# Kernel tuning notes

Measured on AMD Instinct MI355X. Metric: run time of the kernel, lower is better.

The kernel has to match this reference:

```python
import jax, jax.numpy as jnp
import numpy as np

B, C, H, W = 4, 512, 64, 64
CI = C // 8  # q/k channels in spatial attention
EPS = 1e-5


def _conv3(x, w):
    # 3x3 same-padding conv, NCHW / OIHW, no bias (BN follows)
    return jax.lax.conv_general_dilated(x, w, (1, 1), 'SAME',
                                        dimension_numbers=('NCHW', 'OIHW', 'NCHW'))


def _bn_relu(y, g, b, m, v):
    scale = (g / jnp.sqrt(v + EPS))[None, :, None, None]
    return jax.nn.relu((y - m[None, :, None, None]) * scale + b[None, :, None, None])


def setup_inputs() -> dict:
    ks = jax.random.split(jax.random.key(0), 16)
    f = lambda i, sh, s=0.05: jax.random.normal(ks[i], sh, dtype=jnp.float32) * s
    u = lambda i, sh: jax.random.uniform(ks[i], sh, dtype=jnp.float32) + 0.5
    d = {'x': f(0, (B, C, H, W), 1.0)}
    # spatial branch: conv-bn-relu, attention (q/k/v 1x1 convs + alpha), conv-bn-relu
    d['sa_w1'] = f(1, (C, C, 3, 3)); d['sa_g1'] = jnp.ones(C); d['sa_b1'] = jnp.zeros(C)
    d['sa_m1'] = f(2, (C,)); d['sa_v1'] = u(3, (C,))
    d['q_w'] = f(4, (CI, C)); d['q_b'] = jnp.zeros(CI)
    d['k_w'] = f(5, (CI, C)); d['k_b'] = jnp.zeros(CI)
    d['v_w'] = f(6, (C, C)); d['v_b'] = jnp.zeros(C)
    d['alpha'] = jnp.full((1,), 0.1, jnp.float32)
    d['sa_w2'] = f(7, (C, C, 3, 3)); d['sa_g2'] = jnp.ones(C); d['sa_b2'] = jnp.zeros(C)
    d['sa_m2'] = f(8, (C,)); d['sa_v2'] = u(9, (C,))
    # channel branch: conv-bn-relu, channel attention (beta), conv-bn-relu
    d['ca_w1'] = f(10, (C, C, 3, 3)); d['ca_g1'] = jnp.ones(C); d['ca_b1'] = jnp.zeros(C)
    d['ca_m1'] = f(11, (C,)); d['ca_v1'] = u(12, (C,))
    d['beta'] = jnp.full((1,), 0.1, jnp.float32)
    d['ca_w2'] = f(13, (C, C, 3, 3)); d['ca_g2'] = jnp.ones(C); d['ca_b2'] = jnp.zeros(C)
    d['ca_m2'] = f(14, (C,)); d['ca_v2'] = u(15, (C,))
    return d


def reference(x, sa_w1, sa_g1, sa_b1, sa_m1, sa_v1,
              q_w, q_b, k_w, k_b, v_w, v_b, alpha,
              sa_w2, sa_g2, sa_b2, sa_m2, sa_v2,
              ca_w1, ca_g1, ca_b1, ca_m1, ca_v1, beta,
              ca_w2, ca_g2, ca_b2, ca_m2, ca_v2):
    b, c, h, w = x.shape
    # ---- spatial attention branch ----
    s1 = _bn_relu(_conv3(x, sa_w1), sa_g1, sa_b1, sa_m1, sa_v1)
    sf = s1.reshape(b, c, h * w)                      # [B, C, S]
    q = jnp.einsum('oc,bcs->bos', q_w, sf) + q_b[None, :, None]   # [B, C/8, S]
    k = jnp.einsum('oc,bcs->bos', k_w, sf) + k_b[None, :, None]
    v = jnp.einsum('oc,bcs->bos', v_w, sf) + v_b[None, :, None]   # [B, C, S]
    att = jax.nn.softmax(jnp.einsum('bck,bcs->bks', q, k), axis=-1)  # [B, S, S]
    o = jnp.einsum('bcs,bks->bck', v, att).reshape(s1.shape)
    s1 = alpha * o + s1
    sa_out = _bn_relu(_conv3(s1, sa_w2), sa_g2, sa_b2, sa_m2, sa_v2)
    # ---- channel attention branch ----
    c1 = _bn_relu(_conv3(x, ca_w1), ca_g1, ca_b1, ca_m1, ca_v1)
    cf = c1.reshape(b, c, h * w)                      # [B, C, S]
    catt = jax.nn.softmax(jnp.einsum('bcs,bks->bck', cf, cf), axis=-1)  # [B, C, C]
    co = jnp.einsum('bkc,bcs->bks', catt, cf).reshape(c1.shape)
    c1 = beta * co + c1
    ca_out = _bn_relu(_conv3(c1, ca_w2), ca_g2, ca_b2, ca_m2, ca_v2)
    return sa_out + ca_out
```

## Files before the change

kernel.cpp:

```cpp
#include <hip/hip_runtime.h>
#include <hip/hip_bf16.h>

#define EPS_ 1e-5f

typedef __attribute__((ext_vector_type(4))) float f32x4;
typedef __attribute__((ext_vector_type(8))) short s16x8;
typedef unsigned short u16;

__device__ __forceinline__ float bf2f(u16 u) { return __uint_as_float(((unsigned)u) << 16); }
__device__ __forceinline__ u16 f2bf(float f) { __hip_bfloat16 h = __float2bfloat16(f); return *(u16*)&h; }

typedef __attribute__((address_space(3))) unsigned int lds_u32;
typedef const __attribute__((address_space(1))) unsigned int glb_u32;
__device__ __forceinline__ void gload16(const u16* g, u16* l) {
    __builtin_amdgcn_global_load_lds((glb_u32*)g, (lds_u32*)l, 16, 0, 0);
}

__global__ void __launch_bounds__(256) zero_kernel(uint4* __restrict__ p, int n) {
    int i = blockIdx.x * 256 + threadIdx.x;
    if (i < n) p[i] = make_uint4(0, 0, 0, 0);
}

__global__ void __launch_bounds__(256) wpack_kernel(const float* __restrict__ w, u16* __restrict__ wp) {
    int gid = blockIdx.x * 256 + threadIdx.x;
    if (gid >= 9 * 512 * 512) return;
    int tap = gid >> 18, rem = gid & 262143;
    int o = rem >> 9, c = rem & 511;
    wp[gid] = f2bf(w[(o * 512 + c) * 9 + tap]);
}

__global__ void __launch_bounds__(256) cvtb_kernel(const float* __restrict__ a, u16* __restrict__ o, int n) {
    int i = blockIdx.x * 256 + threadIdx.x;
    if (i < n) o[i] = f2bf(a[i]);
}

__global__ void __launch_bounds__(256) tcl_kernel(const float* __restrict__ X, u16* __restrict__ out, int padded) {
    __shared__ float T[64][65];
    const int b = blockIdx.z, y = blockIdx.y, c0 = blockIdx.x * 64;
    const int tid = threadIdx.x;
    const int rr = tid >> 2, q = (tid & 3) * 16;
    const float* src = X + (((size_t)(b * 512 + c0 + rr) * 64 + y) * 64) + q;
#pragma unroll
    for (int i = 0; i < 4; ++i) {
        float4 f = *(const float4*)(src + i * 4);
        T[rr][q + i * 4 + 0] = f.x; T[rr][q + i * 4 + 1] = f.y;
        T[rr][q + i * 4 + 2] = f.z; T[rr][q + i * 4 + 3] = f.w;
    }
    __syncthreads();
    u16 v[16];
#pragma unroll
    for (int i = 0; i < 16; ++i) v[i] = f2bf(T[q + i][rr]);
    u16* dst = padded ? out + ((size_t)((b * 66 + y + 1) * 66 + rr + 1)) * 512 + c0 + q
                      : out + ((size_t)(b * 4096 + y * 64 + rr)) * 512 + c0 + q;
    *(s16x8*)dst       = *(s16x8*)&v[0];
    *(s16x8*)(dst + 8) = *(s16x8*)&v[8];
}

template <int MODE>
__global__ void __launch_bounds__(256) conv_mfma_kernel(
        const u16* __restrict__ Tcl, const u16* __restrict__ Wb,
        const float* __restrict__ gg, const float* __restrict__ bb,
        const float* __restrict__ mn, const float* __restrict__ vr,
        float* __restrict__ Y) {
    __shared__ __align__(16) u16 Ash[4096];
    __shared__ __align__(16) u16 Bsh[4096];
    const int tid = threadIdx.x, lane = tid & 63, wid = tid >> 6;
    const int wm = wid >> 1, wn = wid & 1;
    const int b = blockIdx.z, m0 = blockIdx.y * 128, s0 = blockIdx.x * 128;
    const int y0 = s0 >> 6;

    const int off0 = wid * 1024 + lane * 16;
    const int row0 = off0 >> 6, kb0 = (off0 & 63) >> 1;
    const int x_im = row0 & 63;
    const size_t aoff0 = (size_t)(m0 + row0) * 512 + kb0;
    const size_t aoff1 = aoff0 + (size_t)64 * 512;
    const size_t bbase0 = ((size_t)(b * 66 + y0 + 1) * 66 + x_im + 1) * 512 + kb0;
    const size_t bbase1 = ((size_t)(b * 66 + y0 + 2) * 66 + x_im + 1) * 512 + kb0;
    u16* ldsA0 = Ash + wid * 512; u16* ldsA1 = ldsA0 + 2048;
    u16* ldsB0 = Bsh + wid * 512; u16* ldsB1 = ldsB0 + 2048;

    f32x4 acc[4][4];
#pragma unroll
    for (int i = 0; i < 4; ++i)
#pragma unroll
        for (int j = 0; j < 4; ++j) acc[i][j] = (f32x4){0.f, 0.f, 0.f, 0.f};

    const int ra = wm * 64 + (lane & 15);
    const int rb = wn * 64 + (lane & 15);
    const int kq = (lane >> 4) * 8;

    for (int tap = 0; tap < 9; ++tap) {
        const u16* At = Wb + (size_t)tap * 262144;
        const long bshift = (long)((tap / 3 - 1) * 66 + (tap % 3 - 1)) * 512;
        const u16* Bt0 = Tcl + bbase0 + bshift;
        const u16* Bt1 = Tcl + bbase1 + bshift;
        for (int k0 = 0; k0 < 512; k0 += 32) {
            gload16(At + aoff0 + k0, ldsA0);
            gload16(At + aoff1 + k0, ldsA1);
            gload16(Bt0 + k0, ldsB0);
            gload16(Bt1 + k0, ldsB1);
            __syncthreads();
            s16x8 a[4], bf[4];
#pragma unroll
            for (int i = 0; i < 4; ++i) a[i]  = *(const s16x8*)&Ash[(ra + i * 16) * 32 + kq];
#pragma unroll
            for (int j = 0; j < 4; ++j) bf[j] = *(const s16x8*)&Bsh[(rb + j * 16) * 32 + kq];
#pragma unroll
            for (int i = 0; i < 4; ++i)
#pragma unroll
                for (int j = 0; j < 4; ++j)
                    acc[i][j] = __builtin_amdgcn_mfma_f32_16x16x32_bf16(a[i], bf[j], acc[i][j], 0, 0, 0);
            __syncthreads();
        }
    }

#pragma unroll
    for (int i = 0; i < 4; ++i) {
#pragma unroll
        for (int r = 0; r < 4; ++r) {
            const int c = m0 + wm * 64 + i * 16 + (lane >> 4) * 4 + r;
            const float sc = gg[c] * rsqrtf(vr[c] + EPS_);
            const float bn = bb[c] - mn[c] * sc;
            const size_t rowi = ((size_t)(b * 512 + c)) * 4096;
#pragma unroll
            for (int j = 0; j < 4; ++j) {
                const int s = s0 + wn * 64 + j * 16 + (lane & 15);
                const float v = fmaxf(acc[i][j][r] * sc + bn, 0.f);
                if (MODE == 0) Y[rowi + s] = v;
                else           Y[rowi + s] += v;
            }
        }
    }
}

template <int EPI>
__global__ void __launch_bounds__(256) mfma_nt_kernel(
        const u16* __restrict__ A, int lda, long sA,
        const u16* __restrict__ Bm, int ldb, long sB,
        void* __restrict__ C, int ldc, long sC,
        int K, const float* __restrict__ bias, const float* __restrict__ scalar_p) {
    __shared__ __align__(16) u16 Ash[4096];
    __shared__ __align__(16) u16 Bsh[4096];
    const int tid = threadIdx.x, lane = tid & 63, wid = tid >> 6;
    const int wm = wid >> 1, wn = wid & 1;
    const int m0 = blockIdx.y * 128, n0 = blockIdx.x * 128;
    const u16* Ab = A + (size_t)blockIdx.z * sA;
    const u16* Bb = Bm + (size_t)blockIdx.z * sB;

    const int off0 = wid * 1024 + lane * 16;
    const int row0 = off0 >> 6, kb0 = (off0 & 63) >> 1;
    const size_t aoff0 = (size_t)(m0 + row0) * lda + kb0;
    const size_t aoff1 = aoff0 + (size_t)64 * lda;
    const size_t boff0 = (size_t)(n0 + row0) * ldb + kb0;
    const size_t boff1 = boff0 + (size_t)64 * ldb;
    u16* ldsA0 = Ash + wid * 512; u16* ldsA1 = ldsA0 + 2048;
    u16* ldsB0 = Bsh + wid * 512; u16* ldsB1 = ldsB0 + 2048;

    f32x4 acc[4][4];
#pragma unroll
    for (int i = 0; i < 4; ++i)
#pragma unroll
        for (int j = 0; j < 4; ++j) acc[i][j] = (f32x4){0.f, 0.f, 0.f, 0.f};

    const int ra = wm * 64 + (lane & 15);
    const int rb = wn * 64 + (lane & 15);
    const int kq = (lane >> 4) * 8;

    for (int k0 = 0; k0 < K; k0 += 32) {
        gload16(Ab + aoff0 + k0, ldsA0);
        gload16(Ab + aoff1 + k0, ldsA1);
        gload16(Bb + boff0 + k0, ldsB0);
        gload16(Bb + boff1 + k0, ldsB1);
        __syncthreads();
        s16x8 a[4], bf[4];
#pragma unroll
        for (int i = 0; i < 4; ++i) a[i]  = *(const s16x8*)&Ash[(ra + i * 16) * 32 + kq];
#pragma unroll
        for (int j = 0; j < 4; ++j) bf[j] = *(const s16x8*)&Bsh[(rb + j * 16) * 32 + kq];
#pragma unroll
        for (int i = 0; i < 4; ++i)
#pragma unroll
            for (int j = 0; j < 4; ++j)
                acc[i][j] = __builtin_amdgcn_mfma_f32_16x16x32_bf16(a[i], bf[j], acc[i][j], 0, 0, 0);
        __syncthreads();
    }

#pragma unroll
    for (int i = 0; i < 4; ++i) {
#pragma unroll
        for (int r = 0; r < 4; ++r) {
            const int m = m0 + wm * 64 + i * 16 + (lane >> 4) * 4 + r;
            const float bi = (EPI == 0 && bias) ? bias[m] : 0.f;
#pragma unroll
            for (int j = 0; j < 4; ++j) {
                const int n = n0 + wn * 64 + j * 16 + (lane & 15);
                const size_t idx = (size_t)blockIdx.z * sC + (size_t)m * ldc + n;
                if (EPI == 0)      ((u16*)C)[idx] = f2bf(acc[i][j][r] + bi);
                else if (EPI == 1) ((float*)C)[idx] += scalar_p[0] * acc[i][j][r];
                else               ((float*)C)[idx] = acc[i][j][r];
            }
        }
    }
}

template <int TA, int TB, int EPI>
__global__ void __launch_bounds__(256) gemm_kernel(
                 const float* __restrict__ A, int lda, long sA,
                 const float* __restrict__ B, int ldb, long sB,
                 float* __restrict__ C, int ldc, long sC,
                 int K, const float* __restrict__ bias) {
    __shared__ float As[16][68];
    __shared__ float Bs[16][68];
    const float* Ab = A + (size_t)blockIdx.z * sA;
    const float* Bb = B + (size_t)blockIdx.z * sB;
    const int m0 = blockIdx.y * 64, n0 = blockIdx.x * 64;
    const int tid = threadIdx.x;
    const int tm = tid >> 4, tn = tid & 15;

    float acc[4][4];
#pragma unroll
    for (int i = 0; i < 4; ++i)
#pragma unroll
        for (int j = 0; j < 4; ++j) acc[i][j] = 0.f;

    for (int k0 = 0; k0 < K; k0 += 16) {
        if (TA == 0) {
            int m = tid >> 2, kq = (tid & 3) * 4;
            float4 v = *(const float4*)(Ab + (size_t)(m0 + m) * lda + k0 + kq);
            As[kq + 0][m] = v.x; As[kq + 1][m] = v.y; As[kq + 2][m] = v.z; As[kq + 3][m] = v.w;
        } else {
            int k = tid >> 4, mq = (tid & 15) * 4;
            *(float4*)&As[k][mq] = *(const float4*)(Ab + (size_t)(k0 + k) * lda + m0 + mq);
        }
        if (TB == 0) {
            int k = tid >> 4, nq = (tid & 15) * 4;
            *(float4*)&Bs[k][nq] = *(const float4*)(Bb + (size_t)(k0 + k) * ldb + n0 + nq);
        } else {
            int nn = tid >> 2, kq = (tid & 3) * 4;
            float4 v = *(const float4*)(Bb + (size_t)(n0 + nn) * ldb + k0 + kq);
            Bs[kq + 0][nn] = v.x; Bs[kq + 1][nn] = v.y; Bs[kq + 2][nn] = v.z; Bs[kq + 3][nn] = v.w;
        }
        __syncthreads();
#pragma unroll
        for (int k = 0; k < 16; ++k) {
            float4 a4 = *(const float4*)&As[k][tm * 4];
            float4 b4 = *(const float4*)&Bs[k][tn * 4];
            float a[4] = {a4.x, a4.y, a4.z, a4.w};
            float b[4] = {b4.x, b4.y, b4.z, b4.w};
#pragma unroll
            for (int i = 0; i < 4; ++i)
#pragma unroll
                for (int j = 0; j < 4; ++j) acc[i][j] = fmaf(a[i], b[j], acc[i][j]);
        }
        __syncthreads();
    }

#pragma unroll
    for (int i = 0; i < 4; ++i) {
        const int m = m0 + tm * 4 + i;
        const float bim = (EPI == 0 && bias) ? bias[m] : 0.f;
#pragma unroll
        for (int j = 0; j < 4; ++j) {
            const int n = n0 + tn * 4 + j;
            const size_t idx = (size_t)blockIdx.z * sC + (size_t)m * ldc + n;
            if (EPI == 0) C[idx] = acc[i][j] + bim;
            else          ((u16*)C)[idx] = f2bf(acc[i][j] + (bias ? bias[n] : 0.f));
        }
    }
}

__global__ void __launch_bounds__(256) softmax_att_kernel(u16* __restrict__ P) {
    u16* r = P + (size_t)blockIdx.x * 4096;
    const int tid = threadIdx.x;
    __shared__ float red[4], red2[4];
    float v[16];
    {
        s16x8 h0 = *(const s16x8*)(r + tid * 16);
        s16x8 h1 = *(const s16x8*)(r + tid * 16 + 8);
#pragma unroll
        for (int i = 0; i < 8; ++i) { v[i] = bf2f((u16)h0[i]); v[8 + i] = bf2f((u16)h1[i]); }
    }
    float mx = v[0];
#pragma unroll
    for (int i = 1; i < 16; ++i) mx = fmaxf(mx, v[i]);
    for (int o = 32; o > 0; o >>= 1) mx = fmaxf(mx, __shfl_down(mx, o, 64));
    if ((tid & 63) == 0) red[tid >> 6] = mx;
    __syncthreads();
    mx = fmaxf(fmaxf(red[0], red[1]), fmaxf(red[2], red[3]));
    float s = 0.f;
#pragma unroll
    for (int i = 0; i < 16; ++i) { v[i] = __expf(v[i] - mx); s += v[i]; }
    for (int o = 32; o > 0; o >>= 1) s += __shfl_down(s, o, 64);
    if ((tid & 63) == 0) red2[tid >> 6] = s;
    __syncthreads();
    s = red2[0] + red2[1] + red2[2] + red2[3];
    const float inv = 1.f / s;
    u16 w[16];
#pragma unroll
    for (int i = 0; i < 16; ++i) w[i] = f2bf(v[i] * inv);
    *(s16x8*)(r + tid * 16)     = *(s16x8*)&w[0];
    *(s16x8*)(r + tid * 16 + 8) = *(s16x8*)&w[8];
}

__global__ void __launch_bounds__(256) softmax_g_kernel(const float* __restrict__ G, u16* __restrict__ Gs) {
    const float* r = G + (size_t)blockIdx.x * 512;
    u16* o = Gs + (size_t)blockIdx.x * 512;
    const int tid = threadIdx.x;
    __shared__ float red[4], red2[4];
    float2 v = *(const float2*)(r + tid * 2);
    float mx = fmaxf(v.x, v.y);
    for (int off = 32; off > 0; off >>= 1) mx = fmaxf(mx, __shfl_down(mx, off, 64));
    if ((tid & 63) == 0) red[tid >> 6] = mx;
    __syncthreads();
    mx = fmaxf(fmaxf(red[0], red[1]), fmaxf(red[2], red[3]));
    float e0 = __expf(v.x - mx), e1 = __expf(v.y - mx);
    float s = e0 + e1;
    for (int off = 32; off > 0; off >>= 1) s += __shfl_down(s, off, 64);
    if ((tid & 63) == 0) red2[tid >> 6] = s;
    __syncthreads();
    s = red2[0] + red2[1] + red2[2] + red2[3];
    const float inv = 1.f / s;
    o[tid * 2] = f2bf(e0 * inv);
    o[tid * 2 + 1] = f2bf(e1 * inv);
}

extern "C" void kernel_launch(void* const* d_in, const int* in_sizes, int n_in,
                              void* d_out, int out_size, void* d_ws, size_t ws_size,
                              hipStream_t stream) {
    const float* x     = (const float*)d_in[0];
    const float* sa_w1 = (const float*)d_in[1];
    const float* sa_g1 = (const float*)d_in[2];
    const float* sa_b1 = (const float*)d_in[3];
    const float* sa_m1 = (const float*)d_in[4];
    const float* sa_v1 = (const float*)d_in[5];
    const float* q_w   = (const float*)d_in[6];
    const float* q_b   = (const float*)d_in[7];
    const float* k_w   = (const float*)d_in[8];
    const float* k_b   = (const float*)d_in[9];
    const float* v_w   = (const float*)d_in[10];
    const float* v_b   = (const float*)d_in[11];
    const float* alpha = (const float*)d_in[12];
    const float* sa_w2 = (const float*)d_in[13];
    const float* sa_g2 = (const float*)d_in[14];
    const float* sa_b2 = (const float*)d_in[15];
    const float* sa_m2 = (const float*)d_in[16];
    const float* sa_v2 = (const float*)d_in[17];
    const float* ca_w1 = (const float*)d_in[18];
    const float* ca_g1 = (const float*)d_in[19];
    const float* ca_b1 = (const float*)d_in[20];
    const float* ca_m1 = (const float*)d_in[21];
    const float* ca_v1 = (const float*)d_in[22];
    const float* beta  = (const float*)d_in[23];
    const float* ca_w2 = (const float*)d_in[24];
    const float* ca_g2 = (const float*)d_in[25];
    const float* ca_b2 = (const float*)d_in[26];
    const float* ca_m2 = (const float*)d_in[27];
    const float* ca_v2 = (const float*)d_in[28];

    float* out = (float*)d_out;

    char* wsb = (char*)d_ws;
    float* S1f = (float*)wsb;                 wsb += 8388608ull * 4;
    float* C1f = (float*)wsb;                 wsb += 8388608ull * 4;
    float* G   = (float*)wsb;                 wsb += 1048576ull * 4;
    u16* Tcl   = (u16*)wsb;                   wsb += 8921088ull * 2;
    u16* CLB   = (u16*)wsb;                   wsb += 8388608ull * 2;
    u16* Wb    = (u16*)wsb;                   wsb += 2359296ull * 2;
    u16* VWb   = (u16*)wsb;                   wsb += 262144ull * 2;
    u16* Vb    = (u16*)wsb;                   wsb += 8388608ull * 2;
    u16* ATT   = (u16*)wsb;                   wsb += 16777216ull * 2;
    u16* Gsb   = (u16*)wsb;                   wsb += 1048576ull * 2;
    u16* Qt    = (u16*)wsb;                   wsb += 1048576ull * 2;
    u16* Kt    = (u16*)wsb;                   wsb += 1048576ull * 2;
    u16* C1b   = Vb;

    const long IMG = 512L * 4096;
    dim3 cgrid(32, 4, 4);
    dim3 tgrid(8, 64, 4);

    zero_kernel<<<4357, 256, 0, stream>>>((uint4*)Tcl, 1115136);

    tcl_kernel<<<tgrid, 256, 0, stream>>>(x, Tcl, 1);
    wpack_kernel<<<9216, 256, 0, stream>>>(sa_w1, Wb);
    conv_mfma_kernel<0><<<cgrid, 256, 0, stream>>>(Tcl, Wb, sa_g1, sa_b1, sa_m1, sa_v1, S1f);
    wpack_kernel<<<9216, 256, 0, stream>>>(ca_w1, Wb);
    conv_mfma_kernel<0><<<cgrid, 256, 0, stream>>>(Tcl, Wb, ca_g1, ca_b1, ca_m1, ca_v1, C1f);

    gemm_kernel<1, 1, 3><<<dim3(1, 64, 4), 256, 0, stream>>>(
        S1f, 4096, IMG, q_w, 512, 0, (float*)Qt, 64, 262144, 512, q_b);
    gemm_kernel<1, 1, 3><<<dim3(1, 64, 4), 256, 0, stream>>>(
        S1f, 4096, IMG, k_w, 512, 0, (float*)Kt, 64, 262144, 512, k_b);

    cvtb_kernel<<<1024, 256, 0, stream>>>(v_w, VWb, 262144);
    tcl_kernel<<<tgrid, 256, 0, stream>>>(S1f, CLB, 0);
    mfma_nt_kernel<0><<<dim3(32, 4, 4), 256, 0, stream>>>(
        VWb, 512, 0, CLB, 512, 2097152, Vb, 4096, 2097152, 512, v_b, nullptr);

    for (int b = 0; b < 4; ++b) {
        mfma_nt_kernel<0><<<dim3(32, 32, 1), 256, 0, stream>>>(
            Qt + b * 262144, 64, 0, Kt + b * 262144, 64, 0, ATT, 4096, 0, 64, nullptr, nullptr);
        softmax_att_kernel<<<4096, 256, 0, stream>>>(ATT);
        mfma_nt_kernel<1><<<dim3(32, 4, 1), 256, 0, stream>>>(
            Vb + b * 2097152, 4096, 0, ATT, 4096, 0, S1f + b * IMG, 4096, 0, 4096, nullptr, alpha);
    }

    tcl_kernel<<<tgrid, 256, 0, stream>>>(S1f, Tcl, 1);
    wpack_kernel<<<9216, 256, 0, stream>>>(sa_w2, Wb);
    conv_mfma_kernel<0><<<cgrid, 256, 0, stream>>>(Tcl, Wb, sa_g2, sa_b2, sa_m2, sa_v2, out);

    cvtb_kernel<<<32768, 256, 0, stream>>>(C1f, C1b, 8388608);
    mfma_nt_kernel<2><<<dim3(4, 4, 4), 256, 0, stream>>>(
        C1b, 4096, 2097152, C1b, 4096, 2097152, G, 512, 262144, 4096, nullptr, nullptr);
    softmax_g_kernel<<<2048, 256, 0, stream>>>(G, Gsb);
    tcl_kernel<<<tgrid, 256, 0, stream>>>(C1f, CLB, 0);
    mfma_nt_kernel<1><<<dim3(32, 4, 4), 256, 0, stream>>>(
        Gsb, 512, 262144, CLB, 512, 2097152, C1f, 4096, IMG, 512, nullptr, beta);

    tcl_kernel<<<tgrid, 256, 0, stream>>>(C1f, Tcl, 1);
    wpack_kernel<<<9216, 256, 0, stream>>>(ca_w2, Wb);
    conv_mfma_kernel<2><<<cgrid, 256, 0, stream>>>(Tcl, Wb, ca_g2, ca_b2, ca_m2, ca_v2, out);
}
```

Before: 1.290 ms.

## Fuse Q/K projections into one bf16 MFMA GEMM and swizzle LDS layout

Replaces the two fp32 SIMT gemm_kernel launches for the Q and K 1x1 projections with a single bf16 MFMA GEMM over the channels-last S1 buffer. It writes an interleaved [S,128] QK tensor with per-column bias, and the attention-logit GEMM reads Q and K from it using stride 128. Separately, it adds an XOR swizzle of the k-offset to the LDS staging and fragment reads in both the conv and generic MFMA kernels to reduce LDS bank conflicts. Q/K are now computed from bf16 inputs, which loses some precision, and the swizzle only gives correct results if the write and read XOR patterns match.

```diff
diff --git a/kernel.cpp b/kernel.cpp
--- a/kernel.cpp
+++ b/kernel.cpp
@@ -32,6 +32,12 @@
 __global__ void __launch_bounds__(256) cvtb_kernel(const float* __restrict__ a, u16* __restrict__ o, int n) {
     int i = blockIdx.x * 256 + threadIdx.x;
     if (i < n) o[i] = f2bf(a[i]);
+}
+
+__global__ void qkbias_kernel(const float* __restrict__ qb, const float* __restrict__ kb,
+                              float* __restrict__ o) {
+    int i = threadIdx.x;
+    o[i] = (i < 64) ? qb[i] : kb[i - 64];
 }
 
 __global__ void __launch_bounds__(256) tcl_kernel(const float* __restrict__ X, u16* __restrict__ out, int padded) {
@@ -70,7 +76,8 @@
     const int y0 = s0 >> 6;
 
     const int off0 = wid * 1024 + lane * 16;
-    const int row0 = off0 >> 6, kb0 = (off0 & 63) >> 1;
+    const int row0 = off0 >> 6;
+    const int kb0 = (((off0 & 63) >> 1)) ^ (((lane >> 3) & 3) << 3);
     const int x_im = row0 & 63;
     const size_t aoff0 = (size_t)(m0 + row0) * 512 + kb0;
     const size_t aoff1 = aoff0 + (size_t)64 * 512;
@@ -87,7 +94,7 @@
 
     const int ra = wm * 64 + (lane & 15);
     const int rb = wn * 64 + (lane & 15);
-    const int kq = (lane >> 4) * 8;
+    const int kq = ((lane >> 4) * 8) ^ (((lane >> 1) & 3) << 3);
 
     for (int tap = 0; tap < 9; ++tap) {
         const u16* At = Wb + (size_t)tap * 262144;
@@ -148,7 +155,8 @@
     const u16* Bb = Bm + (size_t)blockIdx.z * sB;
 
     const int off0 = wid * 1024 + lane * 16;
-    const int row0 = off0 >> 6, kb0 = (off0 & 63) >> 1;
+    const int row0 = off0 >> 6;
+    const int kb0 = (((off0 & 63) >> 1)) ^ (((lane >> 3) & 3) << 3);
     const size_t aoff0 = (size_t)(m0 + row0) * lda + kb0;
     const size_t aoff1 = aoff0 + (size_t)64 * lda;
     const size_t boff0 = (size_t)(n0 + row0) * ldb + kb0;
@@ -164,7 +172,7 @@
 
     const int ra = wm * 64 + (lane & 15);
     const int rb = wn * 64 + (lane & 15);
-    const int kq = (lane >> 4) * 8;
+    const int kq = ((lane >> 4) * 8) ^ (((lane >> 1) & 3) << 3);
 
     for (int k0 = 0; k0 < K; k0 += 32) {
         gload16(Ab + aoff0 + k0, ldsA0);
@@ -190,81 +198,16 @@
 #pragma unroll
         for (int r = 0; r < 4; ++r) {
             const int m = m0 + wm * 64 + i * 16 + (lane >> 4) * 4 + r;
-            const float bi = (EPI == 0 && bias) ? bias[m] : 0.f;
+            const float bim = (EPI == 0 && bias) ? bias[m] : 0.f;
 #pragma unroll
             for (int j = 0; j < 4; ++j) {
                 const int n = n0 + wn * 64 + j * 16 + (lane & 15);
                 const size_t idx = (size_t)blockIdx.z * sC + (size_t)m * ldc + n;
-                if (EPI == 0)      ((u16*)C)[idx] = f2bf(acc[i][j][r] + bi);
+                if (EPI == 0)      ((u16*)C)[idx] = f2bf(acc[i][j][r] + bim);
                 else if (EPI == 1) ((float*)C)[idx] += scalar_p[0] * acc[i][j][r];
-                else               ((float*)C)[idx] = acc[i][j][r];
+                else if (EPI == 2) ((float*)C)[idx] = acc[i][j][r];
+                else               ((u16*)C)[idx] = f2bf(acc[i][j][r] + (bias ? bias[n] : 0.f));
             }
-        }
-    }
-}
-
-template <int TA, int TB, int EPI>
-__global__ void __launch_bounds__(256) gemm_kernel(
-                 const float* __restrict__ A, int lda, long sA,
-                 const float* __restrict__ B, int ldb, long sB,
-                 float* __restrict__ C, int ldc, long sC,
-                 int K, const float* __restrict__ bias) {
-    __shared__ float As[16][68];
-    __shared__ float Bs[16][68];
-    const float* Ab = A + (size_t)blockIdx.z * sA;
-    const float* Bb = B + (size_t)blockIdx.z * sB;
-    const int m0 = blockIdx.y * 64, n0 = blockIdx.x * 64;
-    const int tid = threadIdx.x;
-    const int tm = tid >> 4, tn = tid & 15;
-
-    float acc[4][4];
-#pragma unroll
-    for (int i = 0; i < 4; ++i)
-#pragma unroll
-        for (int j = 0; j < 4; ++j) acc[i][j] = 0.f;
-
-    for (int k0 = 0; k0 < K; k0 += 16) {
-        if (TA == 0) {
-            int m = tid >> 2, kq = (tid & 3) * 4;
-            float4 v = *(const float4*)(Ab + (size_t)(m0 + m) * lda + k0 + kq);
-            As[kq + 0][m] = v.x; As[kq + 1][m] = v.y; As[kq + 2][m] = v.z; As[kq + 3][m] = v.w;
-        } else {
-            int k = tid >> 4, mq = (tid & 15) * 4;
-            *(float4*)&As[k][mq] = *(const float4*)(Ab + (size_t)(k0 + k) * lda + m0 + mq);
-        }
-        if (TB == 0) {
-            int k = tid >> 4, nq = (tid & 15) * 4;
-            *(float4*)&Bs[k][nq] = *(const float4*)(Bb + (size_t)(k0 + k) * ldb + n0 + nq);
-        } else {
-            int nn = tid >> 2, kq = (tid & 3) * 4;
-            float4 v = *(const float4*)(Bb + (size_t)(n0 + nn) * ldb + k0 + kq);
-            Bs[kq + 0][nn] = v.x; Bs[kq + 1][nn] = v.y; Bs[kq + 2][nn] = v.z; Bs[kq + 3][nn] = v.w;
-        }
-        __syncthreads();
-#pragma unroll
-        for (int k = 0; k < 16; ++k) {
-            float4 a4 = *(const float4*)&As[k][tm * 4];
-            float4 b4 = *(const float4*)&Bs[k][tn * 4];
-            float a[4] = {a4.x, a4.y, a4.z, a4.w};
-            float b[4] = {b4.x, b4.y, b4.z, b4.w};
-#pragma unroll
-            for (int i = 0; i < 4; ++i)
-#pragma unroll
-                for (int j = 0; j < 4; ++j) acc[i][j] = fmaf(a[i], b[j], acc[i][j]);
-        }
-        __syncthreads();
-    }
-
-#pragma unroll
-    for (int i = 0; i < 4; ++i) {
-        const int m = m0 + tm * 4 + i;
-        const float bim = (EPI == 0 && bias) ? bias[m] : 0.f;
-#pragma unroll
-        for (int j = 0; j < 4; ++j) {
-            const int n = n0 + tn * 4 + j;
-            const size_t idx = (size_t)blockIdx.z * sC + (size_t)m * ldc + n;
-            if (EPI == 0) C[idx] = acc[i][j] + bim;
-            else          ((u16*)C)[idx] = f2bf(acc[i][j] + (bias ? bias[n] : 0.f));
         }
     }
 }
@@ -363,15 +306,16 @@
     float* S1f = (float*)wsb;                 wsb += 8388608ull * 4;
     float* C1f = (float*)wsb;                 wsb += 8388608ull * 4;
     float* G   = (float*)wsb;                 wsb += 1048576ull * 4;
+    float* QKB = (float*)wsb;                 wsb += 128 * 4;
     u16* Tcl   = (u16*)wsb;                   wsb += 8921088ull * 2;
     u16* CLB   = (u16*)wsb;                   wsb += 8388608ull * 2;
     u16* Wb    = (u16*)wsb;                   wsb += 2359296ull * 2;
     u16* VWb   = (u16*)wsb;                   wsb += 262144ull * 2;
+    u16* QKw   = (u16*)wsb;                   wsb += 65536ull * 2;
     u16* Vb    = (u16*)wsb;                   wsb += 8388608ull * 2;
     u16* ATT   = (u16*)wsb;                   wsb += 16777216ull * 2;
     u16* Gsb   = (u16*)wsb;                   wsb += 1048576ull * 2;
-    u16* Qt    = (u16*)wsb;                   wsb += 1048576ull * 2;
-    u16* Kt    = (u16*)wsb;                   wsb += 1048576ull * 2;
+    u16* QKt   = (u16*)wsb;                   wsb += 2097152ull * 2;
     u16* C1b   = Vb;
 
     const long IMG = 512L * 4096;
@@ -386,19 +330,20 @@
     wpack_kernel<<<9216, 256, 0, stream>>>(ca_w1, Wb);
     conv_mfma_kernel<0><<<cgrid, 256, 0, stream>>>(Tcl, Wb, ca_g1, ca_b1, ca_m1, ca_v1, C1f);
 
-    gemm_kernel<1, 1, 3><<<dim3(1, 64, 4), 256, 0, stream>>>(
-        S1f, 4096, IMG, q_w, 512, 0, (float*)Qt, 64, 262144, 512, q_b);
-    gemm_kernel<1, 1, 3><<<dim3(1, 64, 4), 256, 0, stream>>>(
-        S1f, 4096, IMG, k_w, 512, 0, (float*)Kt, 64, 262144, 512, k_b);
-
     cvtb_kernel<<<1024, 256, 0, stream>>>(v_w, VWb, 262144);
+    cvtb_kernel<<<128, 256, 0, stream>>>(q_w, QKw, 32768);
+    cvtb_kernel<<<128, 256, 0, stream>>>(k_w, QKw + 32768, 32768);
+    qkbias_kernel<<<1, 128, 0, stream>>>(q_b, k_b, QKB);
+
     tcl_kernel<<<tgrid, 256, 0, stream>>>(S1f, CLB, 0);
+    mfma_nt_kernel<3><<<dim3(1, 32, 4), 256, 0, stream>>>(
+        CLB, 512, 2097152, QKw, 512, 0, QKt, 128, 524288, 512, QKB, nullptr);
     mfma_nt_kernel<0><<<dim3(32, 4, 4), 256, 0, stream>>>(
         VWb, 512, 0, CLB, 512, 2097152, Vb, 4096, 2097152, 512, v_b, nullptr);
 
     for (int b = 0; b < 4; ++b) {
         mfma_nt_kernel<0><<<dim3(32, 32, 1), 256, 0, stream>>>(
-            Qt + b * 262144, 64, 0, Kt + b * 262144, 64, 0, ATT, 4096, 0, 64, nullptr, nullptr);
+            QKt + b * 524288, 128, 0, QKt + b * 524288 + 64, 128, 0, ATT, 4096, 0, 64, nullptr, nullptr);
         softmax_att_kernel<<<4096, 256, 0, stream>>>(ATT);
         mfma_nt_kernel<1><<<dim3(32, 4, 1), 256, 0, stream>>>(
             Vb + b * 2097152, 4096, 0, ATT, 4096, 0, S1f + b * IMG, 4096, 0, 4096, nullptr, alpha);
```

Measured after the change: 1.222 ms. 5.3% less time.
